# Kernel optimization log

Measured on AMD Instinct MI355X. Metric: run time of the kernel, lower is better.

Reference implementation:

```python
import jax, jax.numpy as jnp
import numpy as np

N_NODES = 50000


def _gcn_norm(edge_index, num_nodes):
    # PyG GCNConv default: add self-loops, symmetric normalization D^-1/2 A D^-1/2
    src, dst = edge_index[0], edge_index[1]
    loops = jnp.arange(num_nodes, dtype=src.dtype)
    src = jnp.concatenate([src, loops])
    dst = jnp.concatenate([dst, loops])
    deg = jax.ops.segment_sum(jnp.ones_like(src, dtype=jnp.float32), dst,
                              num_segments=num_nodes)
    dis = jnp.where(deg > 0, jax.lax.rsqrt(jnp.maximum(deg, 1.0)), 0.0)
    norm = dis[src] * dis[dst]  # [E']
    return src, dst, norm


def _gcn_conv(x, W, b, src, dst, norm, num_nodes):
    h = x @ W                                   # [N, out] transform first
    msg = h[src] * norm[:, None]                # [E', out] gather + scale
    agg = jax.ops.segment_sum(msg, dst, num_segments=num_nodes)  # scatter-add
    return agg + b


def setup_inputs() -> dict:
    key = jax.random.key(0)
    k1, k2, k3, k4 = jax.random.split(key, 4)
    n, e, d_in, d_h = N_NODES, 800000, 256, 128
    basic_block = jax.random.normal(k1, (n, d_in), dtype=jnp.float32)
    edge_index = jax.random.randint(k2, (2, e), 0, n, dtype=jnp.int64)
    W1 = jax.random.normal(k3, (d_in, d_h), dtype=jnp.float32) * (1.0 / np.sqrt(d_in))
    b1 = jnp.zeros((d_h,), dtype=jnp.float32)
    W2 = jax.random.normal(k4, (d_h, d_h), dtype=jnp.float32) * (1.0 / np.sqrt(d_h))
    b2 = jnp.zeros((d_h,), dtype=jnp.float32)
    return {"basic_block": basic_block, "edge_index": edge_index,
            "W1": W1, "b1": b1, "W2": W2, "b2": b2}


def reference(basic_block, edge_index, W1, b1, W2, b2):
    n = basic_block.shape[0]
    src, dst, norm = _gcn_norm(edge_index, n)
    x = jax.nn.relu(_gcn_conv(basic_block, W1, b1, src, dst, norm, n))
    x = _gcn_conv(x, W2, b2, src, dst, norm, n)
    return x
```

## Files before the change

### kernel.cpp

```cpp
#include <hip/hip_runtime.h>
#include <hip/hip_bf16.h>
#include <stdint.h>

#define D_H 128

typedef __bf16 bf16_t;
typedef unsigned short u16;
typedef bf16_t bf16x8 __attribute__((ext_vector_type(8)));
typedef bf16_t bf16x4 __attribute__((ext_vector_type(4)));
typedef float  f32x4  __attribute__((ext_vector_type(4)));

__global__ void k_pre(const int* __restrict__ dst, int* __restrict__ cnt4,
                      u16* __restrict__ rank, int E, int Nn, int gcr,
                      const float* __restrict__ W1, bf16_t* __restrict__ W1h,
                      bf16_t* __restrict__ W1l, int K1,
                      const float* __restrict__ W2, bf16_t* __restrict__ W2h,
                      bf16_t* __restrict__ W2l, int K2) {
    int bx = (int)blockIdx.x;
    if (bx < gcr) {
        int e = bx * 256 + threadIdx.x;
        if (e < E) {
            int d = dst[e];
            rank[e] = (u16)atomicAdd(&cnt4[(bx & 3) * Nn + d], 1);
        }
        return;
    }
    int id = (bx - gcr) * 256 + threadIdx.x;
    int n1 = K1 * 128;
    if (id < n1) {
        int k = id >> 7, n = id & 127;
        float w = W1[id];
        bf16_t h = (bf16_t)w;
        W1h[(size_t)n * K1 + k] = h;
        W1l[(size_t)n * K1 + k] = (bf16_t)(w - (float)h);
    } else if (id < n1 + K2 * 128) {
        int id2 = id - n1;
        int k = id2 >> 7, n = id2 & 127;
        float w = W2[id2];
        bf16_t h = (bf16_t)w;
        W2h[(size_t)n * K2 + k] = h;
        W2l[(size_t)n * K2 + k] = (bf16_t)(w - (float)h);
    }
}

__global__ __launch_bounds__(1024) void k_scan1(const int* __restrict__ cnt4,
                                                int* __restrict__ out,
                                                int* __restrict__ bsums,
                                                float* __restrict__ dis, int N) {
    __shared__ int tmp[1024];
    int t = threadIdx.x;
    int i = blockIdx.x * 1024 + t;
    int v = 0;
    if (i < N) {
        v = cnt4[i] + cnt4[N + i] + cnt4[2 * N + i] + cnt4[3 * N + i];
        dis[i] = 1.0f / sqrtf((float)(v + 1));
    }
    tmp[t] = v;
    __syncthreads();
    for (int d = 1; d < 1024; d <<= 1) {
        int x = (t >= d) ? tmp[t - d] : 0;
        __syncthreads();
        tmp[t] += x;
        __syncthreads();
    }
    if (i < N) out[i] = tmp[t] - v;
    if (t == 1023) bsums[blockIdx.x] = tmp[t];
}

__global__ void k_scan2(int* __restrict__ bsums, int nb) {
    __shared__ int tmp[64];
    int t = threadIdx.x;
    int v = (t < nb) ? bsums[t] : 0;
    tmp[t] = v;
    __syncthreads();
    for (int d = 1; d < 64; d <<= 1) {
        int x = (t >= d) ? tmp[t - d] : 0;
        __syncthreads();
        tmp[t] += x;
        __syncthreads();
    }
    if (t < nb) bsums[t] = tmp[t] - v;
}

__global__ __launch_bounds__(1024) void k_scan3(int* __restrict__ off,
                                                const int* __restrict__ bsums,
                                                const int* __restrict__ cnt4,
                                                int* __restrict__ offc,
                                                int N, int E) {
    int i = blockIdx.x * 1024 + threadIdx.x;
    if (i < N) {
        int o = off[i] + bsums[blockIdx.x];
        off[i] = o;
        int c0 = cnt4[i], c1 = cnt4[N + i], c2 = cnt4[2 * N + i];
        offc[i]         = o;
        offc[N + i]     = o + c0;
        offc[2 * N + i] = o + c0 + c1;
        offc[3 * N + i] = o + c0 + c1 + c2;
    }
    if (i == 0) off[N] = E;
}

#define LDK 40
#define FILL_PER 2

__global__ __launch_bounds__(256) void k_mm1fill(
        const float* __restrict__ Af,
        const bf16_t* __restrict__ Wh, const bf16_t* __restrict__ Wl,
        const float* __restrict__ dis, bf16_t* __restrict__ Cb,
        int N, int K,
        const int* __restrict__ src, const int* __restrict__ dst,
        const int* __restrict__ offc, const u16* __restrict__ rank,
        u16* __restrict__ csr16, int E, int totThreads) {
    __shared__ bf16_t AsH[64][LDK];
    __shared__ bf16_t AsL[64][LDK];
    __shared__ bf16_t BsH[64][LDK];
    __shared__ bf16_t BsL[64][LDK];

    const int t    = threadIdx.x;
    const int lane = t & 63;
    const int wave = t >> 6;
    const int row0 = ((int)blockIdx.x >> 1) * 64;
    const int col0 = ((int)blockIdx.x & 1) * 64;
    const int wm   = (wave & 1) * 32;
    const int wn   = (wave >> 1) * 32;
    const int fm   = lane & 15;
    const int fq   = lane >> 4;

    const int g = (int)blockIdx.x * 256 + t;
    int epos[FILL_PER];
    u16 esrc[FILL_PER];
#pragma unroll
    for (int i = 0; i < FILL_PER; i++) {
        int e = g + i * totThreads;
        if (e < E) {
            int d    = dst[e];
            int copy = (e >> 8) & 3;
            epos[i] = offc[copy * N + d] + (int)rank[e];
            esrc[i] = (u16)src[e];
        } else {
            epos[i] = -1;
            esrc[i] = 0;
        }
    }

    f32x4 acc[2][2] = {};

    for (int k0 = 0; k0 < K; k0 += 32) {
        __syncthreads();
#pragma unroll
        for (int i = 0; i < 2; i++) {
            int idx = t + i * 256;
            int r   = idx >> 3;
            int c4  = idx & 7;
            int gr  = row0 + r;
            float4 v = make_float4(0.f, 0.f, 0.f, 0.f);
            if (gr < N) v = *(const float4*)(Af + (size_t)gr * K + k0 + c4 * 4);
            bf16_t h0 = (bf16_t)v.x, h1 = (bf16_t)v.y, h2 = (bf16_t)v.z, h3 = (bf16_t)v.w;
            bf16_t l0 = (bf16_t)(v.x - (float)h0);
            bf16_t l1 = (bf16_t)(v.y - (float)h1);
            bf16_t l2 = (bf16_t)(v.z - (float)h2);
            bf16_t l3 = (bf16_t)(v.w - (float)h3);
            *(bf16x4*)&AsH[r][c4 * 4] = (bf16x4){h0, h1, h2, h3};
            *(bf16x4*)&AsL[r][c4 * 4] = (bf16x4){l0, l1, l2, l3};
        }
        {
            int r  = t >> 2;
            int c8 = t & 3;
            *(bf16x8*)&BsH[r][c8 * 8] = *(const bf16x8*)(Wh + (size_t)(col0 + r) * K + k0 + c8 * 8);
            *(bf16x8*)&BsL[r][c8 * 8] = *(const bf16x8*)(Wl + (size_t)(col0 + r) * K + k0 + c8 * 8);
        }
        __syncthreads();

        bf16x8 ah[2], al[2], bh[2], bl[2];
#pragma unroll
        for (int i = 0; i < 2; i++) {
            ah[i] = *(const bf16x8*)&AsH[wm + i * 16 + fm][fq * 8];
            al[i] = *(const bf16x8*)&AsL[wm + i * 16 + fm][fq * 8];
            bh[i] = *(const bf16x8*)&BsH[wn + i * 16 + fm][fq * 8];
            bl[i] = *(const bf16x8*)&BsL[wn + i * 16 + fm][fq * 8];
        }
#pragma unroll
        for (int mi = 0; mi < 2; mi++)
#pragma unroll
            for (int ni = 0; ni < 2; ni++) {
                acc[mi][ni] = __builtin_amdgcn_mfma_f32_16x16x32_bf16(ah[mi], bh[ni], acc[mi][ni], 0, 0, 0);
                acc[mi][ni] = __builtin_amdgcn_mfma_f32_16x16x32_bf16(ah[mi], bl[ni], acc[mi][ni], 0, 0, 0);
                acc[mi][ni] = __builtin_amdgcn_mfma_f32_16x16x32_bf16(al[mi], bh[ni], acc[mi][ni], 0, 0, 0);
            }
    }

#pragma unroll
    for (int mi = 0; mi < 2; mi++)
#pragma unroll
        for (int r = 0; r < 4; r++) {
            int grow = row0 + wm + mi * 16 + fq * 4 + r;
            if (grow < N) {
                float dr = dis[grow];
#pragma unroll
                for (int ni = 0; ni < 2; ni++)
                    Cb[(size_t)grow * D_H + col0 + wn + ni * 16 + fm] = (bf16_t)(dr * acc[mi][ni][r]);
            }
        }

#pragma unroll
    for (int i = 0; i < FILL_PER; i++)
        if (epos[i] >= 0) csr16[epos[i]] = esrc[i];
}

__global__ __launch_bounds__(256) void k_mm2(const bf16_t* __restrict__ Ah,
                                             const bf16_t* __restrict__ Al,
                                             const bf16_t* __restrict__ Wh,
                                             const bf16_t* __restrict__ Wl,
                                             const float* __restrict__ dis,
                                             bf16_t* __restrict__ Cb,
                                             int N, int K) {
    __shared__ bf16_t AsH[64][LDK];
    __shared__ bf16_t AsL[64][LDK];
    __shared__ bf16_t BsH[64][LDK];
    __shared__ bf16_t BsL[64][LDK];

    const int t    = threadIdx.x;
    const int lane = t & 63;
    const int wave = t >> 6;
    const int row0 = ((int)blockIdx.x >> 1) * 64;
    const int col0 = ((int)blockIdx.x & 1) * 64;
    const int wm   = (wave & 1) * 32;
    const int wn   = (wave >> 1) * 32;
    const int fm   = lane & 15;
    const int fq   = lane >> 4;

    f32x4 acc[2][2] = {};

    for (int k0 = 0; k0 < K; k0 += 32) {
        __syncthreads();
        {
            int r  = t >> 2;
            int c8 = t & 3;
            int gr = row0 + r;
            bf16x8 vh = {}, vl = {};
            if (gr < N) {
                vh = *(const bf16x8*)(Ah + (size_t)gr * K + k0 + c8 * 8);
                vl = *(const bf16x8*)(Al + (size_t)gr * K + k0 + c8 * 8);
            }
            *(bf16x8*)&AsH[r][c8 * 8] = vh;
            *(bf16x8*)&AsL[r][c8 * 8] = vl;
            *(bf16x8*)&BsH[r][c8 * 8] = *(const bf16x8*)(Wh + (size_t)(col0 + r) * K + k0 + c8 * 8);
            *(bf16x8*)&BsL[r][c8 * 8] = *(const bf16x8*)(Wl + (size_t)(col0 + r) * K + k0 + c8 * 8);
        }
        __syncthreads();

        bf16x8 ah[2], al[2], bh[2], bl[2];
#pragma unroll
        for (int i = 0; i < 2; i++) {
            ah[i] = *(const bf16x8*)&AsH[wm + i * 16 + fm][fq * 8];
            al[i] = *(const bf16x8*)&AsL[wm + i * 16 + fm][fq * 8];
            bh[i] = *(const bf16x8*)&BsH[wn + i * 16 + fm][fq * 8];
            bl[i] = *(const bf16x8*)&BsL[wn + i * 16 + fm][fq * 8];
        }
#pragma unroll
        for (int mi = 0; mi < 2; mi++)
#pragma unroll
            for (int ni = 0; ni < 2; ni++) {
                acc[mi][ni] = __builtin_amdgcn_mfma_f32_16x16x32_bf16(ah[mi], bh[ni], acc[mi][ni], 0, 0, 0);
                acc[mi][ni] = __builtin_amdgcn_mfma_f32_16x16x32_bf16(ah[mi], bl[ni], acc[mi][ni], 0, 0, 0);
                acc[mi][ni] = __builtin_amdgcn_mfma_f32_16x16x32_bf16(al[mi], bh[ni], acc[mi][ni], 0, 0, 0);
            }
    }

#pragma unroll
    for (int mi = 0; mi < 2; mi++)
#pragma unroll
        for (int r = 0; r < 4; r++) {
            int grow = row0 + wm + mi * 16 + fq * 4 + r;
            if (grow < N) {
                float dr = dis[grow];
#pragma unroll
                for (int ni = 0; ni < 2; ni++)
                    Cb[(size_t)grow * D_H + col0 + wn + ni * 16 + fm] = (bf16_t)(dr * acc[mi][ni][r]);
            }
        }
}

__global__ __launch_bounds__(256) void k_agg(const bf16_t* __restrict__ Hb,
                                             const float* __restrict__ dis,
                                             const int* __restrict__ off,
                                             const u16* __restrict__ csr16,
                                             const float4* __restrict__ bias4,
                                             float4* __restrict__ outF,
                                             bf16_t* __restrict__ outH,
                                             bf16_t* __restrict__ outL,
                                             int N, int mode) {
    const int slot = threadIdx.x >> 4;
    const int lane = threadIdx.x & 15;
    const int node = blockIdx.x * 16 + slot;
    if (node >= N) return;

    const bf16_t* Hrow = Hb + (size_t)lane * 8;

    float a0[8], a1[8], a2[8], a3[8];
    {
        bf16x8 v = *(const bf16x8*)(Hrow + (size_t)node * D_H);
#pragma unroll
        for (int j = 0; j < 8; j++) { a0[j] = (float)v[j]; a1[j] = 0.f; a2[j] = 0.f; a3[j] = 0.f; }
    }

    int p  = off[node];
    int p1 = off[node + 1];

    for (; p + 4 <= p1; p += 4) {
        int s0 = (int)csr16[p + 0], s1 = (int)csr16[p + 1];
        int s2 = (int)csr16[p + 2], s3 = (int)csr16[p + 3];
        bf16x8 h0 = *(const bf16x8*)(Hrow + (size_t)s0 * D_H);
        bf16x8 h1 = *(const bf16x8*)(Hrow + (size_t)s1 * D_H);
        bf16x8 h2 = *(const bf16x8*)(Hrow + (size_t)s2 * D_H);
        bf16x8 h3 = *(const bf16x8*)(Hrow + (size_t)s3 * D_H);
#pragma unroll
        for (int j = 0; j < 8; j++) {
            a0[j] += (float)h0[j];
            a1[j] += (float)h1[j];
            a2[j] += (float)h2[j];
            a3[j] += (float)h3[j];
        }
    }
    if (p + 2 <= p1) {
        int s0 = (int)csr16[p + 0], s1 = (int)csr16[p + 1];
        bf16x8 h0 = *(const bf16x8*)(Hrow + (size_t)s0 * D_H);
        bf16x8 h1 = *(const bf16x8*)(Hrow + (size_t)s1 * D_H);
#pragma unroll
        for (int j = 0; j < 8; j++) { a0[j] += (float)h0[j]; a1[j] += (float)h1[j]; }
        p += 2;
    }
    if (p < p1) {
        int s0 = (int)csr16[p];
        bf16x8 h0 = *(const bf16x8*)(Hrow + (size_t)s0 * D_H);
#pragma unroll
        for (int j = 0; j < 8; j++) a2[j] += (float)h0[j];
    }

    float sum[8];
#pragma unroll
    for (int j = 0; j < 8; j++) sum[j] = (a0[j] + a1[j]) + (a2[j] + a3[j]);

    const float  di = dis[node];
    const float4 b0 = bias4[lane * 2];
    const float4 b1 = bias4[lane * 2 + 1];
    float v0 = fmaf(di, sum[0], b0.x), v1 = fmaf(di, sum[1], b0.y);
    float v2 = fmaf(di, sum[2], b0.z), v3 = fmaf(di, sum[3], b0.w);
    float v4 = fmaf(di, sum[4], b1.x), v5 = fmaf(di, sum[5], b1.y);
    float v6 = fmaf(di, sum[6], b1.z), v7 = fmaf(di, sum[7], b1.w);

    if (mode == 1) {
        v0 = fmaxf(v0, 0.f); v1 = fmaxf(v1, 0.f); v2 = fmaxf(v2, 0.f); v3 = fmaxf(v3, 0.f);
        v4 = fmaxf(v4, 0.f); v5 = fmaxf(v5, 0.f); v6 = fmaxf(v6, 0.f); v7 = fmaxf(v7, 0.f);
        bf16_t h0 = (bf16_t)v0, h1 = (bf16_t)v1, h2 = (bf16_t)v2, h3 = (bf16_t)v3;
        bf16_t h4 = (bf16_t)v4, h5 = (bf16_t)v5, h6 = (bf16_t)v6, h7 = (bf16_t)v7;
        *(bf16x8*)(outH + (size_t)node * D_H + lane * 8) =
            (bf16x8){h0, h1, h2, h3, h4, h5, h6, h7};
        *(bf16x8*)(outL + (size_t)node * D_H + lane * 8) =
            (bf16x8){(bf16_t)(v0 - (float)h0), (bf16_t)(v1 - (float)h1),
                     (bf16_t)(v2 - (float)h2), (bf16_t)(v3 - (float)h3),
                     (bf16_t)(v4 - (float)h4), (bf16_t)(v5 - (float)h5),
                     (bf16_t)(v6 - (float)h6), (bf16_t)(v7 - (float)h7)};
    } else {
        outF[(size_t)node * 32 + lane * 2]     = make_float4(v0, v1, v2, v3);
        outF[(size_t)node * 32 + lane * 2 + 1] = make_float4(v4, v5, v6, v7);
    }
}

extern "C" void kernel_launch(void* const* d_in, const int* in_sizes, int n_in,
                              void* d_out, int out_size, void* d_ws, size_t ws_size,
                              hipStream_t stream) {
    const float* X  = (const float*)d_in[0];
    const int*   ei = (const int*)d_in[1];
    const float* W1 = (const float*)d_in[2];
    const float* b1 = (const float*)d_in[3];
    const float* W2 = (const float*)d_in[4];
    const float* b2 = (const float*)d_in[5];
    float* out = (float*)d_out;

    const int N  = in_sizes[0] / 256;
    const int E  = in_sizes[1] / 2;
    const int K1 = 256;

    const int* src = ei;
    const int* dst = ei + E;

    uintptr_t p = (uintptr_t)d_ws;
    auto carve = [&](size_t bytes) {
        uintptr_t q = p;
        p += (bytes + 255) & ~(size_t)255;
        return q;
    };
    int*    cnt4  = (int*)carve((size_t)N * 4 * 4);
    int*    off   = (int*)carve((size_t)(N + 1) * 4);
    int*    offc  = (int*)carve((size_t)N * 4 * 4);
    int*    bsums = (int*)carve(64 * 4);
    float*  dis   = (float*)carve((size_t)N * 4);
    u16*    rank  = (u16*)carve((size_t)E * 2);
    u16*    csr16 = (u16*)carve((size_t)E * 2);
    bf16_t* Hb    = (bf16_t*)carve((size_t)N * D_H * 2);
    bf16_t* X1h   = (bf16_t*)carve((size_t)N * D_H * 2);
    bf16_t* X1l   = (bf16_t*)carve((size_t)N * D_H * 2);
    bf16_t* W1h   = (bf16_t*)carve((size_t)K1 * D_H * 2);
    bf16_t* W1l   = (bf16_t*)carve((size_t)K1 * D_H * 2);
    bf16_t* W2h   = (bf16_t*)carve((size_t)D_H * D_H * 2);
    bf16_t* W2l   = (bf16_t*)carve((size_t)D_H * D_H * 2);

    const int nb = (N + 1023) / 1024;

    hipMemsetAsync(cnt4, 0, (size_t)N * 4 * 4, stream);
    const int gcr = (E + 255) / 256;
    const int gw  = (K1 * 128 + D_H * 128 + 255) / 256;
    k_pre<<<gcr + gw, 256, 0, stream>>>(dst, cnt4, rank, E, N, gcr,
                                        W1, W1h, W1l, K1,
                                        W2, W2h, W2l, D_H);
    k_scan1<<<nb, 1024, 0, stream>>>(cnt4, off, bsums, dis, N);
    k_scan2<<<1, 64, 0, stream>>>(bsums, nb);
    k_scan3<<<nb, 1024, 0, stream>>>(off, bsums, cnt4, offc, N, E);

    const int gmm = ((N + 63) / 64) * 2;
    const int gag = (N + 15) / 16;

    k_mm1fill<<<gmm, 256, 0, stream>>>(X, W1h, W1l, dis, Hb, N, K1,
                                       src, dst, offc, rank, csr16, E, gmm * 256);
    k_agg<<<gag, 256, 0, stream>>>(Hb, dis, off, csr16,
                                   (const float4*)b1, nullptr, X1h, X1l, N, 1);

    k_mm2<<<gmm, 256, 0, stream>>>(X1h, X1l, W2h, W2l, dis, Hb, N, D_H);
    k_agg<<<gag, 256, 0, stream>>>(Hb, dis, off, csr16,
                                   (const float4*)b2, (float4*)out, nullptr, nullptr, N, 0);
}
```

Measured before the change: 250.1 us.

## Fuse degree count and prefix scan into one persistent kernel with grid barriers

Replaces the separate count, three-stage scan kernels with a single persistent kernel of 1024 main blocks that counts destination degrees, then uses spin-wait grid barriers to do block scan, a block-sum scan and the offset write. Weight splitting blocks are appended to the same launch. This removes three kernel launches and their gaps, at the cost of relying on all 1024 main blocks being co-resident; the appended weight blocks are scheduled alongside and could delay or deadlock if residency is insufficient. The memset is extended to zero the barrier counters.

```diff
diff --git a/kernel.cpp b/kernel.cpp
--- a/kernel.cpp
+++ b/kernel.cpp
@@ -10,94 +10,110 @@
 typedef bf16_t bf16x4 __attribute__((ext_vector_type(4)));
 typedef float  f32x4  __attribute__((ext_vector_type(4)));
 
-__global__ void k_pre(const int* __restrict__ dst, int* __restrict__ cnt4,
-                      u16* __restrict__ rank, int E, int Nn, int gcr,
-                      const float* __restrict__ W1, bf16_t* __restrict__ W1h,
-                      bf16_t* __restrict__ W1l, int K1,
-                      const float* __restrict__ W2, bf16_t* __restrict__ W2h,
-                      bf16_t* __restrict__ W2l, int K2) {
-    int bx = (int)blockIdx.x;
-    if (bx < gcr) {
-        int e = bx * 256 + threadIdx.x;
-        if (e < E) {
-            int d = dst[e];
-            rank[e] = (u16)atomicAdd(&cnt4[(bx & 3) * Nn + d], 1);
+#define MAINB 1024
+
+static __device__ __forceinline__ void gridbar(int* ctr, int target) {
+    __syncthreads();
+    if (threadIdx.x == 0) {
+        __threadfence();
+        atomicAdd(ctr, 1);
+        while (atomicAdd(ctr, 0) < target) { }
+        __threadfence();
+    }
+    __syncthreads();
+}
+
+__global__ __launch_bounds__(256) void k_prescan(
+        const int* __restrict__ dst, int* __restrict__ cnt4,
+        u16* __restrict__ rank, int E, int N,
+        int* __restrict__ bars, int* __restrict__ bsums,
+        int* __restrict__ off, int* __restrict__ offc, float* __restrict__ dis,
+        const float* __restrict__ W1, bf16_t* __restrict__ W1h,
+        bf16_t* __restrict__ W1l, int K1,
+        const float* __restrict__ W2, bf16_t* __restrict__ W2h,
+        bf16_t* __restrict__ W2l, int K2, int scanBlks) {
+    const int bx = (int)blockIdx.x;
+    const int t  = threadIdx.x;
+
+    if (bx >= MAINB) {
+        int id = (bx - MAINB) * 256 + t;
+        int n1 = K1 * 128;
+        if (id < n1) {
+            int k = id >> 7, n = id & 127;
+            float w = W1[id];
+            bf16_t h = (bf16_t)w;
+            W1h[(size_t)n * K1 + k] = h;
+            W1l[(size_t)n * K1 + k] = (bf16_t)(w - (float)h);
+        } else if (id < n1 + K2 * 128) {
+            int id2 = id - n1;
+            int k = id2 >> 7, n = id2 & 127;
+            float w = W2[id2];
+            bf16_t h = (bf16_t)w;
+            W2h[(size_t)n * K2 + k] = h;
+            W2l[(size_t)n * K2 + k] = (bf16_t)(w - (float)h);
         }
         return;
     }
-    int id = (bx - gcr) * 256 + threadIdx.x;
-    int n1 = K1 * 128;
-    if (id < n1) {
-        int k = id >> 7, n = id & 127;
-        float w = W1[id];
-        bf16_t h = (bf16_t)w;
-        W1h[(size_t)n * K1 + k] = h;
-        W1l[(size_t)n * K1 + k] = (bf16_t)(w - (float)h);
-    } else if (id < n1 + K2 * 128) {
-        int id2 = id - n1;
-        int k = id2 >> 7, n = id2 & 127;
-        float w = W2[id2];
-        bf16_t h = (bf16_t)w;
-        W2h[(size_t)n * K2 + k] = h;
-        W2l[(size_t)n * K2 + k] = (bf16_t)(w - (float)h);
-    }
-}
-
-__global__ __launch_bounds__(1024) void k_scan1(const int* __restrict__ cnt4,
-                                                int* __restrict__ out,
-                                                int* __restrict__ bsums,
-                                                float* __restrict__ dis, int N) {
-    __shared__ int tmp[1024];
-    int t = threadIdx.x;
-    int i = blockIdx.x * 1024 + t;
-    int v = 0;
-    if (i < N) {
-        v = cnt4[i] + cnt4[N + i] + cnt4[2 * N + i] + cnt4[3 * N + i];
-        dis[i] = 1.0f / sqrtf((float)(v + 1));
+
+    for (int e = bx * 256 + t; e < E; e += MAINB * 256) {
+        int d = dst[e];
+        int copy = (e >> 8) & 3;
+        rank[e] = (u16)atomicAdd(&cnt4[copy * N + d], 1);
+    }
+    gridbar(&bars[0], MAINB);
+
+    __shared__ int tmp[256];
+    const int node = bx * 256 + t;
+    int v = 0, c0 = 0, c1 = 0, c2 = 0;
+    if (bx < scanBlks && node < N) {
+        c0 = cnt4[node];
+        c1 = cnt4[N + node];
+        c2 = cnt4[2 * N + node];
+        int c3 = cnt4[3 * N + node];
+        v = c0 + c1 + c2 + c3;
+        dis[node] = 1.0f / sqrtf((float)(v + 1));
     }
     tmp[t] = v;
     __syncthreads();
-    for (int d = 1; d < 1024; d <<= 1) {
+    for (int d = 1; d < 256; d <<= 1) {
         int x = (t >= d) ? tmp[t - d] : 0;
         __syncthreads();
         tmp[t] += x;
         __syncthreads();
     }
-    if (i < N) out[i] = tmp[t] - v;
-    if (t == 1023) bsums[blockIdx.x] = tmp[t];
-}
-
-__global__ void k_scan2(int* __restrict__ bsums, int nb) {
-    __shared__ int tmp[64];
-    int t = threadIdx.x;
-    int v = (t < nb) ? bsums[t] : 0;
-    tmp[t] = v;
-    __syncthreads();
-    for (int d = 1; d < 64; d <<= 1) {
-        int x = (t >= d) ? tmp[t - d] : 0;
-        __syncthreads();
-        tmp[t] += x;
-        __syncthreads();
-    }
-    if (t < nb) bsums[t] = tmp[t] - v;
-}
-
-__global__ __launch_bounds__(1024) void k_scan3(int* __restrict__ off,
-                                                const int* __restrict__ bsums,
-                                                const int* __restrict__ cnt4,
-                                                int* __restrict__ offc,
-                                                int N, int E) {
-    int i = blockIdx.x * 1024 + threadIdx.x;
-    if (i < N) {
-        int o = off[i] + bsums[blockIdx.x];
-        off[i] = o;
-        int c0 = cnt4[i], c1 = cnt4[N + i], c2 = cnt4[2 * N + i];
-        offc[i]         = o;
-        offc[N + i]     = o + c0;
-        offc[2 * N + i] = o + c0 + c1;
-        offc[3 * N + i] = o + c0 + c1 + c2;
-    }
-    if (i == 0) off[N] = E;
+    const int excl = tmp[t] - v;
+    if (t == 255) bsums[bx] = tmp[255];
+    gridbar(&bars[1], MAINB);
+
+    if (bx == 0) {
+        int b0 = bsums[t * 4 + 0], b1 = bsums[t * 4 + 1];
+        int b2 = bsums[t * 4 + 2], b3 = bsums[t * 4 + 3];
+        int s = b0 + b1 + b2 + b3;
+        tmp[t] = s;
+        __syncthreads();
+        for (int d = 1; d < 256; d <<= 1) {
+            int x = (t >= d) ? tmp[t - d] : 0;
+            __syncthreads();
+            tmp[t] += x;
+            __syncthreads();
+        }
+        int ex = tmp[t] - s;
+        bsums[t * 4 + 0] = ex;
+        bsums[t * 4 + 1] = ex + b0;
+        bsums[t * 4 + 2] = ex + b0 + b1;
+        bsums[t * 4 + 3] = ex + b0 + b1 + b2;
+    }
+    gridbar(&bars[2], MAINB);
+
+    if (bx < scanBlks && node < N) {
+        int o = bsums[bx] + excl;
+        off[node]        = o;
+        offc[node]       = o;
+        offc[N + node]   = o + c0;
+        offc[2 * N + node] = o + c0 + c1;
+        offc[3 * N + node] = o + c0 + c1 + c2;
+    }
+    if (bx == 0 && t == 0) off[N] = E;
 }
 
 #define LDK 40
@@ -392,9 +408,10 @@
         return q;
     };
     int*    cnt4  = (int*)carve((size_t)N * 4 * 4);
+    int*    bars  = (int*)carve(256);
     int*    off   = (int*)carve((size_t)(N + 1) * 4);
     int*    offc  = (int*)carve((size_t)N * 4 * 4);
-    int*    bsums = (int*)carve(64 * 4);
+    int*    bsums = (int*)carve(MAINB * 4);
     float*  dis   = (float*)carve((size_t)N * 4);
     u16*    rank  = (u16*)carve((size_t)E * 2);
     u16*    csr16 = (u16*)carve((size_t)E * 2);
@@ -406,17 +423,14 @@
     bf16_t* W2h   = (bf16_t*)carve((size_t)D_H * D_H * 2);
     bf16_t* W2l   = (bf16_t*)carve((size_t)D_H * D_H * 2);
 
-    const int nb = (N + 1023) / 1024;
-
-    hipMemsetAsync(cnt4, 0, (size_t)N * 4 * 4, stream);
-    const int gcr = (E + 255) / 256;
-    const int gw  = (K1 * 128 + D_H * 128 + 255) / 256;
-    k_pre<<<gcr + gw, 256, 0, stream>>>(dst, cnt4, rank, E, N, gcr,
-                                        W1, W1h, W1l, K1,
-                                        W2, W2h, W2l, D_H);
-    k_scan1<<<nb, 1024, 0, stream>>>(cnt4, off, bsums, dis, N);
-    k_scan2<<<1, 64, 0, stream>>>(bsums, nb);
-    k_scan3<<<nb, 1024, 0, stream>>>(off, bsums, cnt4, offc, N, E);
+    hipMemsetAsync(cnt4, 0, (((size_t)N * 16 + 255) & ~(size_t)255) + 256, stream);
+
+    const int gw       = (K1 * 128 + D_H * 128 + 255) / 256;
+    const int scanBlks = (N + 255) / 256;
+    k_prescan<<<MAINB + gw, 256, 0, stream>>>(dst, cnt4, rank, E, N,
+                                              bars, bsums, off, offc, dis,
+                                              W1, W1h, W1l, K1,
+                                              W2, W2h, W2l, D_H, scanBlks);
 
     const int gmm = ((N + 63) / 64) * 2;
     const int gag = (N + 15) / 16;
```

New measurement: 501.8 us. +100.7%, slower.
